# Optimization experiments

Hardware: AMD Instinct MI355X
Metric: run time of the kernel (lower is better)

The kernel has to match this reference:

```python
import jax, jax.numpy as jnp
import numpy as np

N, E, F, H = 20000, 320000, 128, 256   # nodes, edges, in-features, hidden
M, NQ = 4096, 2048                      # lsq rows, QP variables
LAMB_MAX = 2.0


def setup_inputs() -> dict:
    key = jax.random.key(0)
    ks = jax.random.split(key, 12)
    x = jax.random.normal(ks[0], (N, F), jnp.float32)
    edge_index = jax.random.randint(ks[1], (2, E), 0, N)
    A = jax.random.normal(ks[2], (M, NQ), jnp.float32) * 0.05
    b = jax.random.normal(ks[3], (M, 1), jnp.float32)
    feat_ids = jax.random.randint(ks[4], (NQ,), 0, N)
    x_prior = jax.random.uniform(ks[5], (NQ, 1), jnp.float32)
    lamb = jnp.ones((1,), jnp.float32)
    # ChebConv K=2 weights: one linear per Chebyshev order, plus bias
    W10 = jax.random.normal(ks[6], (F, H), jnp.float32) / np.sqrt(F)
    W11 = jax.random.normal(ks[7], (F, H), jnp.float32) / np.sqrt(F)
    b1 = jnp.zeros((H,), jnp.float32)
    W20 = jax.random.normal(ks[8], (H, 1), jnp.float32) / np.sqrt(H)
    W21 = jax.random.normal(ks[9], (H, 1), jnp.float32) / np.sqrt(H)
    b2 = jnp.zeros((1,), jnp.float32)
    return {"x": x, "edge_index": edge_index, "A": A, "b": b,
            "feat_ids": feat_ids, "x_prior": x_prior, "lamb": lamb,
            "W10": W10, "W11": W11, "b1": b1,
            "W20": W20, "W21": W21, "b2": b2}


def _cheb_conv(x, edge_index, W0, W1, bias, lam_max):
    """PyG ChebConv with K=2: out = x @ W0 + (2L/lam_max - I) x @ W1 + bias,
    L = I - D^{-1/2} A D^{-1/2}, via edge gather/scatter (no dense NxN)."""
    row, col = edge_index[0], edge_index[1]
    n = x.shape[0]
    deg = jax.ops.segment_sum(jnp.ones_like(row, dtype=x.dtype), row, num_segments=n)
    dinv = jnp.where(deg > 0, deg ** -0.5, 0.0)
    # normalized edge weight scaled by 2/lam_max, negated (off-diag of L_hat)
    w = -(2.0 / lam_max) * dinv[row] * dinv[col]              # [E]
    msg = jax.ops.segment_sum(w[:, None] * x[col], row, num_segments=n)
    Tx1 = msg + (2.0 / lam_max - 1.0) * x                      # diagonal of L_hat
    return x @ W0 + Tx1 @ W1 + bias


def reference(x, edge_index, A, b, feat_ids, x_prior, lamb,
              W10, W11, b1, W20, W21, b2):
    h = jax.nn.relu(_cheb_conv(x, edge_index, W10, W11, b1, LAMB_MAX))
    h = lamb[0] * jax.nn.relu(_cheb_conv(h, edge_index, W20, W21, b2, LAMB_MAX))
    hfold = h[feat_ids] + 1e-5                                 # [NQ, 1]
    q = hfold[:, 0]
    # QP: min 1/2 z^T Q z + p^T z with vacuous inequality (0*z <= 0.1) and no
    # equality constraints -> interior-point converges to unconstrained min.
    Q = A.T @ A + jnp.diag(q)                                  # [NQ, NQ]
    p = -(x_prior * hfold)[:, 0] - (b.T @ A)[0]                # [NQ]
    z = jnp.linalg.solve(Q, -p)                                # [NQ]
    return z[:, None]                                          # f.T -> [NQ, 1]
```

## Files before the change

### kernel.cpp

```cpp
#include <hip/hip_runtime.h>

#define N_NODES 20000
#define N_EDGES 320000
#define F_DIM   128
#define H_DIM   256
#define M_ROWS  4096
#define NQ      2048
#define NIT     18
#define MM_ROWS 20032

typedef __attribute__((ext_vector_type(8))) short short8;
typedef __attribute__((ext_vector_type(4))) float f32x4;


__device__ __forceinline__ float wred(float v) {
#pragma unroll
  for (int m = 32; m > 0; m >>= 1) v += __shfl_xor(v, m, 64);
  return v;
}

__device__ __forceinline__ float bred256(float v, float* lds) {
  v = wred(v);
  int w = threadIdx.x >> 6;
  if ((threadIdx.x & 63) == 0) lds[w] = v;
  __syncthreads();
  float tot = lds[0] + lds[1] + lds[2] + lds[3];
  __syncthreads();
  return tot;
}

__device__ __forceinline__ unsigned f2bf(float f) {
  unsigned u = __float_as_uint(f);
  unsigned r = u + 0x7fffu + ((u >> 16) & 1u);
  return r >> 16;
}
__device__ __forceinline__ float bflo(unsigned u) { return __uint_as_float(u << 16); }
__device__ __forceinline__ float bfhi(unsigned u) { return __uint_as_float(u & 0xffff0000u); }


__global__ __launch_bounds__(256) void k_deg(const int* __restrict__ ei, int* __restrict__ deg) {
  int e = blockIdx.x * 256 + threadIdx.x;
  if (e < N_EDGES) atomicAdd(&deg[ei[e]], 1);
}

__global__ __launch_bounds__(1024) void k_scan(const int* __restrict__ deg,
    int* __restrict__ rowstart, float* __restrict__ dinv) {
  __shared__ int part[1024];
  int t = threadIdx.x;
  const int chunk = (N_NODES + 1023) / 1024;
  int lo = t * chunk;
  int hi = lo + chunk; if (hi > N_NODES) hi = N_NODES;
  int s = 0;
  for (int i = lo; i < hi; ++i) {
    int d = deg[i];
    dinv[i] = d > 0 ? rsqrtf((float)d) : 0.f;
    s += d;
  }
  part[t] = s;
  __syncthreads();
  for (int off = 1; off < 1024; off <<= 1) {
    int v = part[t];
    int add = (t >= off) ? part[t - off] : 0;
    __syncthreads();
    part[t] = v + add;
    __syncthreads();
  }
  int base = (t > 0) ? part[t - 1] : 0;
  for (int i = lo; i < hi; ++i) { rowstart[i] = base; base += deg[i]; }
  if (t == 0) rowstart[N_NODES] = part[1023];
}

__global__ __launch_bounds__(256) void k_scatter(const int* __restrict__ ei,
    const int* __restrict__ rowstart, int* __restrict__ cursor,
    const float* __restrict__ dinv, int* __restrict__ cols, float* __restrict__ wvals) {
  int e = blockIdx.x * 256 + threadIdx.x;
  if (e >= N_EDGES) return;
  int r = ei[e];
  int c = ei[N_EDGES + e];
  int pos = rowstart[r] + atomicAdd(&cursor[r], 1);
  cols[pos] = c;
  wvals[pos] = -dinv[r] * dinv[c];
}

#define CONVX_BLKS (MM_ROWS * 16 / 256)

__global__ __launch_bounds__(256) void k_pack(const float* __restrict__ x,
    const float* __restrict__ W10, const float* __restrict__ W11,
    unsigned* __restrict__ xu, unsigned* __restrict__ Wtb) {
  int bx = blockIdx.x;
  if (bx < CONVX_BLKS) {
    int gid = bx * 256 + threadIdx.x;
    int row = gid >> 4;
    int q8 = gid & 15;
    uint4* xu4 = (uint4*)xu;
    if (row < N_NODES) {
      const float4* x4 = (const float4*)x;
      float4 a = x4[(size_t)row * 32 + q8 * 2];
      float4 b = x4[(size_t)row * 32 + q8 * 2 + 1];
      uint4 u;
      u.x = f2bf(a.x) | (f2bf(a.y) << 16);
      u.y = f2bf(a.z) | (f2bf(a.w) << 16);
      u.z = f2bf(b.x) | (f2bf(b.y) << 16);
      u.w = f2bf(b.z) | (f2bf(b.w) << 16);
      xu4[(size_t)row * 32 + q8] = u;
    } else {
      uint4 z = make_uint4(0, 0, 0, 0);
      xu4[(size_t)row * 32 + q8] = z;
      xu4[(size_t)row * 32 + 16 + q8] = z;
    }
  } else {
    int gid = (bx - CONVX_BLKS) * 256 + threadIdx.x;
    int n = gid >> 7;
    int u = gid & 127;
    int k0 = u * 2;
    float v0 = (k0 < 128) ? W10[(size_t)k0 * H_DIM + n]
                          : W11[(size_t)(k0 - 128) * H_DIM + n];
    float v1 = (k0 + 1 < 128) ? W10[(size_t)(k0 + 1) * H_DIM + n]
                              : W11[(size_t)(k0 - 127) * H_DIM + n];
    Wtb[(size_t)n * 128 + u] = f2bf(v0) | (f2bf(v1) << 16);
  }
}

__global__ __launch_bounds__(256) void k_msg1(const int* __restrict__ rowstart,
    const int* __restrict__ cols, const float* __restrict__ wvals,
    unsigned* __restrict__ xu) {
  int wid = (blockIdx.x * 256 + threadIdx.x) >> 6;
  int lane = threadIdx.x & 63;
  if (wid >= N_NODES) return;
  int s0 = rowstart[wid], s1 = rowstart[wid + 1];
  float2 acc = make_float2(0.f, 0.f);
  for (int e = s0; e < s1; ++e) {
    int c = cols[e];
    float w = wvals[e];
    unsigned u = xu[(size_t)c * 128 + lane];
    acc.x += w * bflo(u);
    acc.y += w * bfhi(u);
  }
  xu[(size_t)wid * 128 + 64 + lane] = f2bf(acc.x) | (f2bf(acc.y) << 16);
}


__device__ __forceinline__ void mm_ldfrag(short8* Af, short8* Bf,
    const unsigned* __restrict__ xurow, const unsigned* __restrict__ wrow, int kc) {
#pragma unroll
  for (int a = 0; a < 4; ++a)
    Af[a] = *(const short8*)(xurow + (size_t)a * 16 * 128 + kc * 16);
#pragma unroll
  for (int n = 0; n < 4; ++n)
    Bf[n] = *(const short8*)(wrow + (size_t)n * 16 * 128 + kc * 16);
}

__global__ __launch_bounds__(256) void k_mm(const unsigned* __restrict__ xu,
    const unsigned* __restrict__ Wtb, const float* __restrict__ b1,
    const float* __restrict__ W20, const float* __restrict__ W21,
    float* __restrict__ t, float* __restrict__ s) {
  const int row0 = blockIdx.x * 64;
  const int tid = threadIdx.x;
  const int w = tid >> 6, lane = tid & 63;
  const int colb = w * 64;
  const int frow = lane & 15, fqo = (lane >> 4) * 4;
  const int c16 = lane & 15, q4 = lane >> 4;

  f32x4 acc[4][4];
#pragma unroll
  for (int a = 0; a < 4; ++a)
#pragma unroll
    for (int b = 0; b < 4; ++b) {
      acc[a][b][0] = 0.f; acc[a][b][1] = 0.f;
      acc[a][b][2] = 0.f; acc[a][b][3] = 0.f;
    }

  const unsigned* xurow = xu + (size_t)(row0 + frow) * 128 + fqo;
  const unsigned* wrow  = Wtb + (size_t)(colb + frow) * 128 + fqo;

  short8 A0[4], B0[4], A1[4], B1[4];
  mm_ldfrag(A0, B0, xurow, wrow, 0);
#pragma unroll
  for (int kp = 0; kp < 4; ++kp) {
    const int kc = kp * 2;
    mm_ldfrag(A1, B1, xurow, wrow, kc + 1);
#pragma unroll
    for (int a = 0; a < 4; ++a)
#pragma unroll
      for (int n = 0; n < 4; ++n)
        acc[a][n] = __builtin_amdgcn_mfma_f32_16x16x32_bf16(A0[a], B0[n], acc[a][n], 0, 0, 0);
    if (kc + 2 < 8) mm_ldfrag(A0, B0, xurow, wrow, kc + 2);
#pragma unroll
    for (int a = 0; a < 4; ++a)
#pragma unroll
      for (int n = 0; n < 4; ++n)
        acc[a][n] = __builtin_amdgcn_mfma_f32_16x16x32_bf16(A1[a], B1[n], acc[a][n], 0, 0, 0);
  }

  float tp[4][4] = {}, sp[4][4] = {};
#pragma unroll
  for (int b2 = 0; b2 < 4; ++b2) {
    int gc = colb + b2 * 16 + c16;
    float w20 = W20[gc], w21 = W21[gc], bb = b1[gc];
#pragma unroll
    for (int a = 0; a < 4; ++a)
#pragma unroll
      for (int r = 0; r < 4; ++r) {
        float val = acc[a][b2][r] + bb;
        val = val > 0.f ? val : 0.f;
        tp[a][r] += val * w20;
        sp[a][r] += val * w21;
      }
  }
#pragma unroll
  for (int a = 0; a < 4; ++a)
#pragma unroll
    for (int r = 0; r < 4; ++r) {
#pragma unroll
      for (int m = 1; m < 16; m <<= 1) {
        tp[a][r] += __shfl_xor(tp[a][r], m, 64);
        sp[a][r] += __shfl_xor(sp[a][r], m, 64);
      }
    }
  if (c16 == 0) {
#pragma unroll
    for (int a = 0; a < 4; ++a)
#pragma unroll
      for (int r = 0; r < 4; ++r) {
        int gr = row0 + a * 16 + q4 * 4 + r;
        if (gr < N_NODES) {
          atomicAdd(&t[gr], tp[a][r]);
          atomicAdd(&s[gr], sp[a][r]);
        }
      }
  }
}


__global__ __launch_bounds__(256) void k_h2(const float* __restrict__ t,
    const float* __restrict__ s, const int* __restrict__ rowstart,
    const int* __restrict__ cols, const float* __restrict__ wvals,
    const float* __restrict__ lamb, const float* __restrict__ b2, float* __restrict__ h2) {
  int i = blockIdx.x * 256 + threadIdx.x;
  if (i >= N_NODES) return;
  float m = 0.f;
  int s0 = rowstart[i], s1 = rowstart[i + 1];
  for (int e = s0; e < s1; ++e) m += wvals[e] * s[cols[e]];
  float val = t[i] + m + b2[0];
  val = val > 0.f ? val : 0.f;
  h2[i] = lamb[0] * val;
}

__global__ __launch_bounds__(256) void k_prep(const float* __restrict__ A,
    const float* __restrict__ b, unsigned* __restrict__ Atu, float* __restrict__ btA_parts) {
  int jp = blockIdx.x * 256 + threadIdx.x;
  int k0 = blockIdx.y * 128;
  const float2* A2 = (const float2*)A;
  float acc0 = 0.f, acc1 = 0.f;
  for (int kk = 0; kk < 128; kk += 8) {
    float ax[8], ay[8];
#pragma unroll
    for (int i = 0; i < 8; ++i) {
      int k = k0 + kk + i;
      float2 a = A2[(size_t)k * 1024 + jp];
      float bk = b[k];
      acc0 += a.x * bk;
      acc1 += a.y * bk;
      ax[i] = a.x; ay[i] = a.y;
    }
    uint4 t0, t1;
    t0.x = f2bf(ax[0]) | (f2bf(ax[1]) << 16);
    t0.y = f2bf(ax[2]) | (f2bf(ax[3]) << 16);
    t0.z = f2bf(ax[4]) | (f2bf(ax[5]) << 16);
    t0.w = f2bf(ax[6]) | (f2bf(ax[7]) << 16);
    t1.x = f2bf(ay[0]) | (f2bf(ay[1]) << 16);
    t1.y = f2bf(ay[2]) | (f2bf(ay[3]) << 16);
    t1.z = f2bf(ay[4]) | (f2bf(ay[5]) << 16);
    t1.w = f2bf(ay[6]) | (f2bf(ay[7]) << 16);
    int uoff = (k0 + kk) >> 1;
    *(uint4*)(Atu + (size_t)(2 * jp) * 2048 + uoff) = t0;
    *(uint4*)(Atu + (size_t)(2 * jp + 1) * 2048 + uoff) = t1;
  }
  ((float2*)(btA_parts + (size_t)blockIdx.y * NQ))[jp] = make_float2(acc0, acc1);
}

__global__ __launch_bounds__(256) void k_qrhs(const float* __restrict__ h2,
    const int* __restrict__ feat_ids, const float* __restrict__ x_prior,
    const float* __restrict__ btA_parts, float* __restrict__ q, float* __restrict__ r) {
  int j = blockIdx.x * 256 + threadIdx.x;
  int f = feat_ids[j];
  float hf = h2[f] + 1e-5f;
  q[j] = hf;
  float bta = 0.f;
#pragma unroll
  for (int c = 0; c < 32; ++c) bta += btA_parts[(size_t)c * NQ + j];
  r[j] = x_prior[j] * hf + bta;
}

#define GR_ST 20
#define NTILE 136

__global__ __launch_bounds__(256) void k_gram(const unsigned* __restrict__ Atu,
                                              float* __restrict__ Gp) {
  __shared__ unsigned shA[128 * GR_ST];
  __shared__ unsigned shB[128 * GR_ST];
  const int bid = blockIdx.x;
  const int wid = (bid & 7) * 68 + (bid >> 3);
  const int tile = wid >> 2;
  const int kq = wid & 3;
  int uu = tile, bi = 0;
  while (uu >= 16 - bi) { uu -= 16 - bi; ++bi; }
  const int bj = bi + uu;
  const int i0 = bi * 128, j0 = bj * 128;
  const int tid = threadIdx.x;
  const int w = tid >> 6, lane = tid & 63;
  const int wr = (w >> 1) * 64, wc = (w & 1) * 64;
  const int srow = tid >> 1, suo = (tid & 1) * 8;
  const int frow = lane & 15, fqo = (lane >> 4) * 4;

  f32x4 acc[4][4];
#pragma unroll
  for (int a = 0; a < 4; ++a)
#pragma unroll
    for (int b = 0; b < 4; ++b) {
      acc[a][b][0] = 0.f; acc[a][b][1] = 0.f;
      acc[a][b][2] = 0.f; acc[a][b][3] = 0.f;
    }

  const unsigned* pa = Atu + (size_t)(i0 + srow) * 2048 + kq * 512 + suo;
  const unsigned* pb = Atu + (size_t)(j0 + srow) * 2048 + kq * 512 + suo;

  uint4 ra0 = *(const uint4*)(pa);
  uint4 ra1 = *(const uint4*)(pa + 4);
  uint4 rb0 = *(const uint4*)(pb);
  uint4 rb1 = *(const uint4*)(pb + 4);

  unsigned* as = shA + srow * GR_ST + suo;
  unsigned* bs = shB + srow * GR_ST + suo;

  for (int si = 0; si < 32; ++si) {
    *(uint4*)as = ra0; *(uint4*)(as + 4) = ra1;
    *(uint4*)bs = rb0; *(uint4*)(bs + 4) = rb1;
    if (si + 1 < 32) {
      const int ku = (si + 1) * 16;
      ra0 = *(const uint4*)(pa + ku);
      ra1 = *(const uint4*)(pa + ku + 4);
      rb0 = *(const uint4*)(pb + ku);
      rb1 = *(const uint4*)(pb + ku + 4);
    }
    __syncthreads();
    short8 af[4], bf[4];
#pragma unroll
    for (int a = 0; a < 4; ++a)
      af[a] = *(const short8*)(shA + (wr + a * 16 + frow) * GR_ST + fqo);
#pragma unroll
    for (int b2 = 0; b2 < 4; ++b2)
      bf[b2] = *(const short8*)(shB + (wc + b2 * 16 + frow) * GR_ST + fqo);
#pragma unroll
    for (int a = 0; a < 4; ++a)
#pragma unroll
      for (int b2 = 0; b2 < 4; ++b2)
        acc[a][b2] = __builtin_amdgcn_mfma_f32_16x16x32_bf16(af[a], bf[b2], acc[a][b2], 0, 0, 0);
    __syncthreads();
  }

  const int q4 = lane >> 4, c16 = lane & 15;
  float* Gz = Gp + ((size_t)kq * NTILE + tile) * 16384;
#pragma unroll
  for (int a = 0; a < 4; ++a)
#pragma unroll
    for (int b2 = 0; b2 < 4; ++b2)
#pragma unroll
      for (int r = 0; r < 4; ++r) {
        int lr = wr + a * 16 + q4 * 4 + r;
        int lc = wc + b2 * 16 + c16;
        Gz[lr * 128 + lc] = acc[a][b2][r];
      }
}

#define GT_ST 131

__global__ __launch_bounds__(256) void k_gconv(const float* __restrict__ Gp,
    const float* __restrict__ q, unsigned* __restrict__ Gb, float* __restrict__ qcorr) {
  __shared__ unsigned short T[128 * GT_ST];
  int uu = blockIdx.x, bi = 0;
  while (uu >= 16 - bi) { uu -= 16 - bi; ++bi; }
  const int bj = bi + uu;
  const int tid = threadIdx.x;
  const int r = tid >> 1, ch = (tid & 1) * 64;
  const size_t tile = (size_t)blockIdx.x * 16384;
  const float4* P0 = (const float4*)(Gp + tile + r * 128 + ch);
  const float4* P1 = (const float4*)(Gp + (size_t)1 * NTILE * 16384 + tile + r * 128 + ch);
  const float4* P2 = (const float4*)(Gp + (size_t)2 * NTILE * 16384 + tile + r * 128 + ch);
  const float4* P3 = (const float4*)(Gp + (size_t)3 * NTILE * 16384 + tile + r * 128 + ch);
  const int gr = bi * 128 + r;
  const bool hasdiag = (bi == bj) && (r >= ch) && (r < ch + 64);
  unsigned uo[32];
#pragma unroll
  for (int j = 0; j < 16; ++j) {
    float4 a = P0[j], b = P1[j], c = P2[j], d = P3[j];
    float v0 = a.x + b.x + c.x + d.x;
    float v1 = a.y + b.y + c.y + d.y;
    float v2 = a.z + b.z + c.z + d.z;
    float v3 = a.w + b.w + c.w + d.w;
    const int c0 = ch + j * 4;
    if (hasdiag && (r - c0 >= 0) && (r - c0 < 4)) {
      float qv = q[gr];
      int dsel = r - c0;
      if (dsel == 0) v0 += qv;
      else if (dsel == 1) v1 += qv;
      else if (dsel == 2) v2 += qv;
      else v3 += qv;
      float vd = (dsel == 0) ? v0 : (dsel == 1) ? v1 : (dsel == 2) ? v2 : v3;
      qcorr[gr] = vd - bflo(f2bf(vd));
    }
    unsigned u0 = f2bf(v0) | (f2bf(v1) << 16);
    unsigned u1 = f2bf(v2) | (f2bf(v3) << 16);
    uo[2 * j] = u0;
    uo[2 * j + 1] = u1;
    T[r * GT_ST + c0]     = (unsigned short)(u0 & 0xffffu);
    T[r * GT_ST + c0 + 1] = (unsigned short)(u0 >> 16);
    T[r * GT_ST + c0 + 2] = (unsigned short)(u1 & 0xffffu);
    T[r * GT_ST + c0 + 3] = (unsigned short)(u1 >> 16);
  }
  uint4* dst = (uint4*)(Gb + (size_t)gr * 1024 + bj * 64 + (ch >> 1));
#pragma unroll
  for (int j = 0; j < 8; ++j) dst[j] = ((const uint4*)uo)[j];
  __syncthreads();
  if (bi != bj) {
    const int wv = tid >> 6, lane = tid & 63;
    for (int kk = 0; kk < 32; ++kk) {
      int rr = kk * 4 + wv;
      unsigned lo = T[(2 * lane) * GT_ST + rr];
      unsigned hi = T[(2 * lane + 1) * GT_ST + rr];
      Gb[(size_t)(bj * 128 + rr) * 1024 + bi * 64 + lane] = lo | (hi << 16);
    }
  }
}

__global__ __launch_bounds__(256) void k_cgG(int k, const unsigned* __restrict__ Gb,
    const float* __restrict__ qcorr,
    const float* __restrict__ r_old, float* __restrict__ r_new,
    const float* __restrict__ p_old, float* __restrict__ p_new,
    const float* __restrict__ Qp_in, float* __restrict__ Qp_out,
    float* __restrict__ xcg) {
  __shared__ float pshare[NQ];
  __shared__ float lds[4];
  const int tid = threadIdx.x, bid = blockIdx.x;
  const float4* r4 = (const float4*)r_old;
  float4 ra = r4[tid * 2], rb2 = r4[tid * 2 + 1];
  float pv[8];
  if (k == 0) {
    pv[0] = ra.x; pv[1] = ra.y; pv[2] = ra.z; pv[3] = ra.w;
    pv[4] = rb2.x; pv[5] = rb2.y; pv[6] = rb2.z; pv[7] = rb2.w;
    if (bid == 0) {
      ((float4*)p_new)[tid * 2] = ra;
      ((float4*)p_new)[tid * 2 + 1] = rb2;
    }
  } else {
    const float4* p4 = (const float4*)p_old;
    const float4* qp4 = (const float4*)Qp_in;
    float4 pa = p4[tid * 2], pb = p4[tid * 2 + 1];
    float4 qa = qp4[tid * 2], qb = qp4[tid * 2 + 1];
    float rr = ra.x * ra.x + ra.y * ra.y + ra.z * ra.z + ra.w * ra.w +
               rb2.x * rb2.x + rb2.y * rb2.y + rb2.z * rb2.z + rb2.w * rb2.w;
    float pap = pa.x * qa.x + pa.y * qa.y + pa.z * qa.z + pa.w * qa.w +
                pb.x * qb.x + pb.y * qb.y + pb.z * qb.z + pb.w * qb.w;
    rr = bred256(rr, lds);
    pap = bred256(pap, lds);
    float alpha = rr / pap;
    if (bid == 0) {
      float4* x4 = (float4*)xcg;
      float4 xa = x4[tid * 2], xb = x4[tid * 2 + 1];
      xa.x += alpha * pa.x; xa.y += alpha * pa.y;
      xa.z += alpha * pa.z; xa.w += alpha * pa.w;
      xb.x += alpha * pb.x; xb.y += alpha * pb.y;
      xb.z += alpha * pb.z; xb.w += alpha * pb.w;
      x4[tid * 2] = xa; x4[tid * 2 + 1] = xb;
    }
    ra.x -= alpha * qa.x; ra.y -= alpha * qa.y;
    ra.z -= alpha * qa.z; ra.w -= alpha * qa.w;
    rb2.x -= alpha * qb.x; rb2.y -= alpha * qb.y;
    rb2.z -= alpha * qb.z; rb2.w -= alpha * qb.w;
    float rrn = ra.x * ra.x + ra.y * ra.y + ra.z * ra.z + ra.w * ra.w +
                rb2.x * rb2.x + rb2.y * rb2.y + rb2.z * rb2.z + rb2.w * rb2.w;
    rrn = bred256(rrn, lds);
    float beta = rrn / rr;
    pv[0] = ra.x + beta * pa.x; pv[1] = ra.y + beta * pa.y;
    pv[2] = ra.z + beta * pa.z; pv[3] = ra.w + beta * pa.w;
    pv[4] = rb2.x + beta * pb.x; pv[5] = rb2.y + beta * pb.y;
    pv[6] = rb2.z + beta * pb.z; pv[7] = rb2.w + beta * pb.w;
    if (bid == 0) {
      ((float4*)r_new)[tid * 2] = ra;
      ((float4*)r_new)[tid * 2 + 1] = rb2;
      ((float4*)p_new)[tid * 2] = make_float4(pv[0], pv[1], pv[2], pv[3]);
      ((float4*)p_new)[tid * 2 + 1] = make_float4(pv[4], pv[5], pv[6], pv[7]);
    }
  }
  ((float4*)pshare)[tid * 2] = make_float4(pv[0], pv[1], pv[2], pv[3]);
  ((float4*)pshare)[tid * 2 + 1] = make_float4(pv[4], pv[5], pv[6], pv[7]);
  __syncthreads();
  const int w = tid >> 6, lane = tid & 63;
  const int row = bid * 4 + w;
  const uint4* Gr = (const uint4*)(Gb + (size_t)row * 1024);
  const float4* ps4 = (const float4*)pshare;
  float acc = 0.f;
#pragma unroll
  for (int c = 0; c < 4; ++c) {
    uint4 gv = Gr[c * 64 + lane];
    float4 pa = ps4[c * 128 + lane * 2];
    float4 pb = ps4[c * 128 + lane * 2 + 1];
    acc += bflo(gv.x) * pa.x + bfhi(gv.x) * pa.y;
    acc += bflo(gv.y) * pa.z + bfhi(gv.y) * pa.w;
    acc += bflo(gv.z) * pb.x + bfhi(gv.z) * pb.y;
    acc += bflo(gv.w) * pb.z + bfhi(gv.w) * pb.w;
  }
  acc = wred(acc);
  if (lane == 0) Qp_out[row] = acc + qcorr[row] * pshare[row];
}

__global__ __launch_bounds__(256) void k_cgfin(const float* __restrict__ r_last,
    const float* __restrict__ p_last, const float* __restrict__ Qp,
    const float* __restrict__ xcg, float* __restrict__ out) {
  const int tid = threadIdx.x;
  const int lane = tid & 63;
  const float4* r4 = (const float4*)r_last;
  const float4* p4 = (const float4*)p_last;
  const float4* q4 = (const float4*)Qp;
  float rr = 0.f, pap = 0.f;
#pragma unroll
  for (int c = 0; c < 4; ++c) {
#pragma unroll
    for (int hh = 0; hh < 2; ++hh) {
      float4 rv = r4[c * 128 + lane * 2 + hh];
      float4 pv = p4[c * 128 + lane * 2 + hh];
      float4 qv = q4[c * 128 + lane * 2 + hh];
      rr += rv.x * rv.x + rv.y * rv.y + rv.z * rv.z + rv.w * rv.w;
      pap += pv.x * qv.x + pv.y * qv.y + pv.z * qv.z + pv.w * qv.w;
    }
  }
  rr = wred(rr);
  pap = wred(pap);
  float alpha = rr / pap;
  const float4* x4 = (const float4*)xcg;
  float4* o4 = (float4*)out;
#pragma unroll
  for (int hh = 0; hh < 2; ++hh) {
    int i4 = tid * 2 + hh;
    float4 xv = x4[i4];
    float4 pv = p4[i4];
    xv.x += alpha * pv.x; xv.y += alpha * pv.y;
    xv.z += alpha * pv.z; xv.w += alpha * pv.w;
    o4[i4] = xv;
  }
}


extern "C" void kernel_launch(void* const* d_in, const int* in_sizes, int n_in,
                              void* d_out, int out_size, void* d_ws, size_t ws_size,
                              hipStream_t stream) {
  const float* x      = (const float*)d_in[0];
  const int*   ei     = (const int*)d_in[1];
  const float* A      = (const float*)d_in[2];
  const float* b      = (const float*)d_in[3];
  const int*   fids   = (const int*)d_in[4];
  const float* xprior = (const float*)d_in[5];
  const float* lamb   = (const float*)d_in[6];
  const float* W10    = (const float*)d_in[7];
  const float* W11    = (const float*)d_in[8];
  const float* b1     = (const float*)d_in[9];
  const float* W20    = (const float*)d_in[10];
  const float* W21    = (const float*)d_in[11];
  const float* b2     = (const float*)d_in[12];
  float* out = (float*)d_out;

  char* base = (char*)d_ws;
  size_t o = 0;
  auto alloc = [&](size_t bytes) { size_t r = o; o = (o + bytes + 255) & ~size_t(255); return r; };

  size_t off_deg    = alloc(N_NODES * 4);
  size_t off_cursor = alloc(N_NODES * 4);
  size_t off_xcg    = alloc(NQ * 4);
  size_t off_t      = alloc(N_NODES * 4);
  size_t off_s      = alloc(N_NODES * 4);
  size_t zero_end   = o;
  size_t off_rowst  = alloc((N_NODES + 1) * 4);
  size_t off_dinv   = alloc(N_NODES * 4);
  size_t off_h2     = alloc(N_NODES * 4);
  size_t off_q      = alloc(NQ * 4);
  size_t off_r0     = alloc(NQ * 4);
  size_t off_r1     = alloc(NQ * 4);
  size_t off_p0     = alloc(NQ * 4);
  size_t off_p1     = alloc(NQ * 4);
  size_t off_Qp0    = alloc(NQ * 4);
  size_t off_Qp1    = alloc(NQ * 4);
  size_t off_qcorr  = alloc(NQ * 4);
  size_t off_btAp   = alloc(32 * NQ * 4);
  size_t off_Wtb    = alloc(256 * 128 * 4);
  size_t sz_cols  = (size_t)N_EDGES * 4 + 256;
  size_t sz_wvals = (size_t)N_EDGES * 4 + 256;
  size_t sz_xmsg  = (size_t)MM_ROWS * 256 * 2;
  size_t union_gnn = sz_cols + sz_wvals + sz_xmsg;
  size_t union_at  = (size_t)M_ROWS * NQ * 2;
  size_t off_union = alloc(union_gnn > union_at ? union_gnn : union_at);
  size_t off_Gp    = alloc((size_t)4 * NTILE * 16384 * 4);
  if (o > ws_size) return;

  int*   deg      = (int*)(base + off_deg);
  int*   cursor   = (int*)(base + off_cursor);
  float* xcg      = (float*)(base + off_xcg);
  float* t        = (float*)(base + off_t);
  float* s        = (float*)(base + off_s);
  int*   rowstart = (int*)(base + off_rowst);
  float* dinv     = (float*)(base + off_dinv);
  float* h2       = (float*)(base + off_h2);
  float* q        = (float*)(base + off_q);
  float* rb[2]    = {(float*)(base + off_r0), (float*)(base + off_r1)};
  float* pg[2]    = {(float*)(base + off_p0), (float*)(base + off_p1)};
  float* Qpb[2]   = {(float*)(base + off_Qp0), (float*)(base + off_Qp1)};
  float* qcorr    = (float*)(base + off_qcorr);
  float* btA_parts = (float*)(base + off_btAp);
  unsigned* Wtb   = (unsigned*)(base + off_Wtb);
  int*   cols     = (int*)(base + off_union);
  float* wvals    = (float*)(base + off_union + sz_cols);
  unsigned* xmsgb = (unsigned*)(base + off_union + sz_cols + sz_wvals);
  unsigned* Atu   = (unsigned*)(base + off_union);
  unsigned* Gb    = (unsigned*)(base + off_union);
  float* Gp       = (float*)(base + off_Gp);

  hipMemsetAsync(d_ws, 0, zero_end, stream);

  k_deg<<<(N_EDGES + 255) / 256, 256, 0, stream>>>(ei, deg);
  k_scan<<<1, 1024, 0, stream>>>(deg, rowstart, dinv);
  k_scatter<<<(N_EDGES + 255) / 256, 256, 0, stream>>>(ei, rowstart, cursor, dinv, cols, wvals);

  k_pack<<<CONVX_BLKS + 128, 256, 0, stream>>>(x, W10, W11, xmsgb, Wtb);
  k_msg1<<<N_NODES / 4, 256, 0, stream>>>(rowstart, cols, wvals, xmsgb);
  k_mm<<<MM_ROWS / 64, 256, 0, stream>>>(xmsgb, Wtb, b1, W20, W21, t, s);
  k_h2<<<(N_NODES + 255) / 256, 256, 0, stream>>>(t, s, rowstart, cols, wvals, lamb, b2, h2);

  k_prep<<<dim3(4, 32), 256, 0, stream>>>(A, b, Atu, btA_parts);
  k_qrhs<<<NQ / 256, 256, 0, stream>>>(h2, fids, xprior, btA_parts, q, rb[0]);
  k_gram<<<544, 256, 0, stream>>>(Atu, Gp);
  k_gconv<<<NTILE, 256, 0, stream>>>(Gp, q, Gb, qcorr);

  k_cgG<<<512, 256, 0, stream>>>(0, Gb, qcorr, rb[0], rb[0], pg[0], pg[0],
                                 Qpb[1], Qpb[0], xcg);
  for (int k = 1; k < NIT; ++k) {
    k_cgG<<<512, 256, 0, stream>>>(k, Gb, qcorr, rb[(k - 1) & 1], rb[k & 1],
                                   pg[(k - 1) & 1], pg[k & 1],
                                   Qpb[(k - 1) & 1], Qpb[k & 1], xcg);
  }
  k_cgfin<<<1, 256, 0, stream>>>(rb[(NIT - 1) & 1], pg[(NIT - 1) & 1],
                                 Qpb[(NIT - 1) & 1], xcg, out);
}
```

Before: 403.7 us.

## Use 512-thread gram blocks and two rows per wave in CG matvec

The gram kernel moves from 4 to 8 waves per block. Each wave now owns a 64x32 sub-tile, and each thread stages one uint4 per operand instead of two, so per-thread registers drop and more waves hide latency. The CG matvec kernel has each wave compute two rows of G·p and is launched with half as many blocks. This amortizes the per-block CG vector update and reduction work, which every block repeats, at the cost of fewer blocks to cover the bandwidth-bound matvec.

```diff
diff --git a/kernel.cpp b/kernel.cpp
--- a/kernel.cpp
+++ b/kernel.cpp
@@ -295,7 +295,7 @@
 #define GR_ST 20
 #define NTILE 136
 
-__global__ __launch_bounds__(256) void k_gram(const unsigned* __restrict__ Atu,
+__global__ __launch_bounds__(512) void k_gram(const unsigned* __restrict__ Atu,
                                               float* __restrict__ Gp) {
   __shared__ unsigned shA[128 * GR_ST];
   __shared__ unsigned shB[128 * GR_ST];
@@ -309,15 +309,15 @@
   const int i0 = bi * 128, j0 = bj * 128;
   const int tid = threadIdx.x;
   const int w = tid >> 6, lane = tid & 63;
-  const int wr = (w >> 1) * 64, wc = (w & 1) * 64;
-  const int srow = tid >> 1, suo = (tid & 1) * 8;
+  const int wr = (w >> 2) * 64, wc = (w & 3) * 32;
+  const int srow = tid >> 2, suo = (tid & 3) * 4;
   const int frow = lane & 15, fqo = (lane >> 4) * 4;
 
-  f32x4 acc[4][4];
+  f32x4 acc[4][2];
 #pragma unroll
   for (int a = 0; a < 4; ++a)
 #pragma unroll
-    for (int b = 0; b < 4; ++b) {
+    for (int b = 0; b < 2; ++b) {
       acc[a][b][0] = 0.f; acc[a][b][1] = 0.f;
       acc[a][b][2] = 0.f; acc[a][b][3] = 0.f;
     }
@@ -325,36 +325,32 @@
   const unsigned* pa = Atu + (size_t)(i0 + srow) * 2048 + kq * 512 + suo;
   const unsigned* pb = Atu + (size_t)(j0 + srow) * 2048 + kq * 512 + suo;
 
-  uint4 ra0 = *(const uint4*)(pa);
-  uint4 ra1 = *(const uint4*)(pa + 4);
-  uint4 rb0 = *(const uint4*)(pb);
-  uint4 rb1 = *(const uint4*)(pb + 4);
+  uint4 ra = *(const uint4*)(pa);
+  uint4 rb = *(const uint4*)(pb);
 
   unsigned* as = shA + srow * GR_ST + suo;
   unsigned* bs = shB + srow * GR_ST + suo;
 
   for (int si = 0; si < 32; ++si) {
-    *(uint4*)as = ra0; *(uint4*)(as + 4) = ra1;
-    *(uint4*)bs = rb0; *(uint4*)(bs + 4) = rb1;
+    *(uint4*)as = ra;
+    *(uint4*)bs = rb;
     if (si + 1 < 32) {
       const int ku = (si + 1) * 16;
-      ra0 = *(const uint4*)(pa + ku);
-      ra1 = *(const uint4*)(pa + ku + 4);
-      rb0 = *(const uint4*)(pb + ku);
-      rb1 = *(const uint4*)(pb + ku + 4);
+      ra = *(const uint4*)(pa + ku);
+      rb = *(const uint4*)(pb + ku);
     }
     __syncthreads();
-    short8 af[4], bf[4];
+    short8 af[4], bf[2];
 #pragma unroll
     for (int a = 0; a < 4; ++a)
       af[a] = *(const short8*)(shA + (wr + a * 16 + frow) * GR_ST + fqo);
 #pragma unroll
-    for (int b2 = 0; b2 < 4; ++b2)
+    for (int b2 = 0; b2 < 2; ++b2)
       bf[b2] = *(const short8*)(shB + (wc + b2 * 16 + frow) * GR_ST + fqo);
 #pragma unroll
     for (int a = 0; a < 4; ++a)
 #pragma unroll
-      for (int b2 = 0; b2 < 4; ++b2)
+      for (int b2 = 0; b2 < 2; ++b2)
         acc[a][b2] = __builtin_amdgcn_mfma_f32_16x16x32_bf16(af[a], bf[b2], acc[a][b2], 0, 0, 0);
     __syncthreads();
   }
@@ -364,7 +360,7 @@
 #pragma unroll
   for (int a = 0; a < 4; ++a)
 #pragma unroll
-    for (int b2 = 0; b2 < 4; ++b2)
+    for (int b2 = 0; b2 < 2; ++b2)
 #pragma unroll
       for (int r = 0; r < 4; ++r) {
         int lr = wr + a * 16 + q4 * 4 + r;
@@ -496,22 +492,32 @@
   ((float4*)pshare)[tid * 2 + 1] = make_float4(pv[4], pv[5], pv[6], pv[7]);
   __syncthreads();
   const int w = tid >> 6, lane = tid & 63;
-  const int row = bid * 4 + w;
-  const uint4* Gr = (const uint4*)(Gb + (size_t)row * 1024);
+  const int row0 = bid * 8 + w * 2;
+  const uint4* Gr0 = (const uint4*)(Gb + (size_t)row0 * 1024);
+  const uint4* Gr1 = (const uint4*)(Gb + (size_t)(row0 + 1) * 1024);
   const float4* ps4 = (const float4*)pshare;
-  float acc = 0.f;
+  float acc0 = 0.f, acc1 = 0.f;
 #pragma unroll
   for (int c = 0; c < 4; ++c) {
-    uint4 gv = Gr[c * 64 + lane];
+    uint4 g0 = Gr0[c * 64 + lane];
+    uint4 g1 = Gr1[c * 64 + lane];
     float4 pa = ps4[c * 128 + lane * 2];
     float4 pb = ps4[c * 128 + lane * 2 + 1];
-    acc += bflo(gv.x) * pa.x + bfhi(gv.x) * pa.y;
-    acc += bflo(gv.y) * pa.z + bfhi(gv.y) * pa.w;
-    acc += bflo(gv.z) * pb.x + bfhi(gv.z) * pb.y;
-    acc += bflo(gv.w) * pb.z + bfhi(gv.w) * pb.w;
-  }
-  acc = wred(acc);
-  if (lane == 0) Qp_out[row] = acc + qcorr[row] * pshare[row];
+    acc0 += bflo(g0.x) * pa.x + bfhi(g0.x) * pa.y;
+    acc0 += bflo(g0.y) * pa.z + bfhi(g0.y) * pa.w;
+    acc0 += bflo(g0.z) * pb.x + bfhi(g0.z) * pb.y;
+    acc0 += bflo(g0.w) * pb.z + bfhi(g0.w) * pb.w;
+    acc1 += bflo(g1.x) * pa.x + bfhi(g1.x) * pa.y;
+    acc1 += bflo(g1.y) * pa.z + bfhi(g1.y) * pa.w;
+    acc1 += bflo(g1.z) * pb.x + bfhi(g1.z) * pb.y;
+    acc1 += bflo(g1.w) * pb.z + bfhi(g1.w) * pb.w;
+  }
+  acc0 = wred(acc0);
+  acc1 = wred(acc1);
+  if (lane == 0) {
+    Qp_out[row0] = acc0 + qcorr[row0] * pshare[row0];
+    Qp_out[row0 + 1] = acc1 + qcorr[row0 + 1] * pshare[row0 + 1];
+  }
 }
 
 __global__ __launch_bounds__(256) void k_cgfin(const float* __restrict__ r_last,
@@ -636,13 +642,13 @@
 
   k_prep<<<dim3(4, 32), 256, 0, stream>>>(A, b, Atu, btA_parts);
   k_qrhs<<<NQ / 256, 256, 0, stream>>>(h2, fids, xprior, btA_parts, q, rb[0]);
-  k_gram<<<544, 256, 0, stream>>>(Atu, Gp);
+  k_gram<<<544, 512, 0, stream>>>(Atu, Gp);
   k_gconv<<<NTILE, 256, 0, stream>>>(Gp, q, Gb, qcorr);
 
-  k_cgG<<<512, 256, 0, stream>>>(0, Gb, qcorr, rb[0], rb[0], pg[0], pg[0],
+  k_cgG<<<256, 256, 0, stream>>>(0, Gb, qcorr, rb[0], rb[0], pg[0], pg[0],
                                  Qpb[1], Qpb[0], xcg);
   for (int k = 1; k < NIT; ++k) {
-    k_cgG<<<512, 256, 0, stream>>>(k, Gb, qcorr, rb[(k - 1) & 1], rb[k & 1],
+    k_cgG<<<256, 256, 0, stream>>>(k, Gb, qcorr, rb[(k - 1) & 1], rb[k & 1],
                                    pg[(k - 1) & 1], pg[k & 1],
                                    Qpb[(k - 1) & 1], Qpb[k & 1], xcg);
   }
```

Result: no change. 400.5 us (-0.8%).
